# Kernel tuning notes

Measured on AMD Instinct MI355X. Metric: run time of the kernel, lower is better.

Reference implementation:

```python
import jax, jax.numpy as jnp
import numpy as np

TEMPERATURE = 0.5
NEG_FILL = -9e15


def setup_inputs() -> dict:
    key = jax.random.key(0)
    k1, k2 = jax.random.split(key)
    B, D = 8192, 128
    z1 = jax.random.normal(k1, (B, D), dtype=jnp.float32)
    z2 = jax.random.normal(k2, (B, D), dtype=jnp.float32)
    return {"z1": z1, "z2": z2}


def reference(z1, z2):
    B = z1.shape[0]
    N = 2 * B
    z = jnp.concatenate([z1, z2], axis=0)              # [N, D]
    sim = jnp.matmul(z, z.T) / TEMPERATURE             # [N, N]
    eye = jnp.eye(N, dtype=bool)
    sim = jnp.where(eye, NEG_FILL, sim)
    idx = jnp.arange(N)
    pos_idx = (idx + B) % N
    positives = sim[idx, pos_idx]                      # [N]
    loss = -positives + jax.scipy.special.logsumexp(sim, axis=1)
    return loss.mean()
```

## Files before the change

### kernel.cpp

```cpp
#include <hip/hip_runtime.h>
#include <stdint.h>


typedef __attribute__((ext_vector_type(8))) short s16x8;
typedef __attribute__((ext_vector_type(16))) float f32x16;

#define N_TOT   16384
#define NHALF   8192
#define DDIM    128
#define NQ      16
#define QW      (N_TOT / NQ)
#define BN      64
#define NT      (QW / BN)
#define BM      256
#define NRB     (N_TOT / BM)
#define CSH     128.0f
#define LN2     0.69314718055994530942f
#define BF_SCALE 1.6986436f

__device__ __forceinline__ unsigned short f2bf(float f) {
    union { float f; unsigned int u; } v; v.f = f;
    unsigned int u = v.u;
    unsigned int r = (u + 0x7FFFu + ((u >> 16) & 1u)) >> 16;
    return (unsigned short)r;
}

__device__ __forceinline__ void gload_lds16(const void* g, void* l) {
    __builtin_amdgcn_global_load_lds(
        (const __attribute__((address_space(1))) void*)g,
        (__attribute__((address_space(3))) void*)l, 16, 0, 0);
}

__global__ __launch_bounds__(256) void k_castpos(const float* __restrict__ z1,
                                                 const float* __restrict__ z2,
                                                 unsigned short* __restrict__ zb,
                                                 float* __restrict__ pos_part) {
    __shared__ float red[4];
    int i = blockIdx.x * 256 + threadIdx.x;
    float4 a = ((const float4*)z1)[i];
    float4 b = ((const float4*)z2)[i];
    ushort4 oa, ob;
    oa.x = f2bf(a.x * BF_SCALE); oa.y = f2bf(a.y * BF_SCALE);
    oa.z = f2bf(a.z * BF_SCALE); oa.w = f2bf(a.w * BF_SCALE);
    ob.x = f2bf(b.x * BF_SCALE); ob.y = f2bf(b.y * BF_SCALE);
    ob.z = f2bf(b.z * BF_SCALE); ob.w = f2bf(b.w * BF_SCALE);
    ((ushort4*)zb)[i] = oa;
    ((ushort4*)(zb + (size_t)NHALF * DDIM))[i] = ob;
    float s = a.x * b.x + a.y * b.y + a.z * b.z + a.w * b.w;
    for (int o = 32; o; o >>= 1) s += __shfl_xor(s, o);
    int lane = threadIdx.x & 63, w = threadIdx.x >> 6;
    if (lane == 0) red[w] = s;
    __syncthreads();
    if (threadIdx.x == 0) pos_part[blockIdx.x] = red[0] + red[1] + red[2] + red[3];
}

__global__ __launch_bounds__(256) void k_main(const unsigned short* __restrict__ zb,
                                              float* __restrict__ ps) {
    __shared__ s16x8 tile[2][BN * 16];

    const int tid  = threadIdx.x;
    const int lane = tid & 63;
    const int w    = tid >> 6;
    const int h    = lane >> 5;
    const int l31  = lane & 31;

    const int bid = blockIdx.x;
    const int q   = bid >> 6;
    const int rb  = bid & 63;
    const int rowB     = rb * BM + w * 64;
    const int colStart = q * QW;

    s16x8 rf0[8], rf1[8];
    {
        const s16x8* rp0 = (const s16x8*)(zb + (size_t)(rowB + l31) * DDIM);
        const s16x8* rp1 = (const s16x8*)(zb + (size_t)(rowB + 32 + l31) * DDIM);
        #pragma unroll
        for (int ks = 0; ks < 8; ++ks) { rf0[ks] = rp0[ks * 2 + h]; rf1[ks] = rp1[ks * 2 + h]; }
    }

    int soff[4];
    #pragma unroll
    for (int j = 0; j < 4; ++j) {
        int e = w * 4 + j;
        int col = e * 4 + (lane >> 4);
        int chunk = (lane & 15) ^ (col & 15);
        soff[j] = col * 256 + chunk * 16;
    }

    #pragma unroll
    for (int j = 0; j < 4; ++j)
        gload_lds16((const char*)zb + (size_t)colStart * 256 + soff[j],
                    (char*)(&tile[0][0]) + (w * 4 + j) * 1024);
    #pragma unroll
    for (int j = 0; j < 4; ++j)
        gload_lds16((const char*)zb + (size_t)(colStart + BN) * 256 + soff[j],
                    (char*)(&tile[1][0]) + (w * 4 + j) * 1024);

    float sa[4] = {0.f, 0.f, 0.f, 0.f};
    float sb[4] = {0.f, 0.f, 0.f, 0.f};

    for (int t = 0; t < NT; ++t) {
        if (t == NT - 1) asm volatile("s_waitcnt vmcnt(0)" ::: "memory");
        else             asm volatile("s_waitcnt vmcnt(4)" ::: "memory");
        __builtin_amdgcn_s_barrier();
        const int buf = t & 1;
        const int colBase = colStart + t * BN;
        #pragma unroll
        for (int sdx = 0; sdx < 2; ++sdx) {
            const int c  = sdx * 32 + l31;
            const int cx = c & 15;
            const s16x8* tb = &tile[buf][c * 16];
            s16x8 a[8];
            #pragma unroll
            for (int ks = 0; ks < 8; ++ks) a[ks] = tb[(ks * 2 + h) ^ cx];
            f32x16 acc0 = {-CSH, -CSH, -CSH, -CSH, -CSH, -CSH, -CSH, -CSH,
                           -CSH, -CSH, -CSH, -CSH, -CSH, -CSH, -CSH, -CSH};
            f32x16 acc1 = acc0;
            #pragma unroll
            for (int ks = 0; ks < 8; ++ks) {
                acc0 = __builtin_amdgcn_mfma_f32_32x32x16_bf16(a[ks], rf0[ks], acc0, 0, 0, 0);
                acc1 = __builtin_amdgcn_mfma_f32_32x32x16_bf16(a[ks], rf1[ks], acc1, 0, 0, 0);
            }
            const int cb = colBase + sdx * 32;
            if (cb == rowB) {
                #pragma unroll
                for (int r2 = 0; r2 < 16; ++r2) {
                    int crow = (r2 & 3) + 8 * (r2 >> 2) + 4 * h;
                    if (crow == l31) acc0[r2] = -1e30f;
                }
            }
            if (cb == rowB + 32) {
                #pragma unroll
                for (int r2 = 0; r2 < 16; ++r2) {
                    int crow = (r2 & 3) + 8 * (r2 >> 2) + 4 * h;
                    if (crow == l31) acc1[r2] = -1e30f;
                }
            }
            #pragma unroll
            for (int r2 = 0; r2 < 16; r2 += 4) {
                sa[0] += __builtin_amdgcn_exp2f(acc0[r2 + 0]);
                sa[1] += __builtin_amdgcn_exp2f(acc0[r2 + 1]);
                sa[2] += __builtin_amdgcn_exp2f(acc0[r2 + 2]);
                sa[3] += __builtin_amdgcn_exp2f(acc0[r2 + 3]);
                sb[0] += __builtin_amdgcn_exp2f(acc1[r2 + 0]);
                sb[1] += __builtin_amdgcn_exp2f(acc1[r2 + 1]);
                sb[2] += __builtin_amdgcn_exp2f(acc1[r2 + 2]);
                sb[3] += __builtin_amdgcn_exp2f(acc1[r2 + 3]);
            }
        }
        __builtin_amdgcn_s_barrier();
        if (t + 2 < NT) {
            #pragma unroll
            for (int j = 0; j < 4; ++j)
                gload_lds16((const char*)zb + (size_t)(colBase + 2 * BN) * 256 + soff[j],
                            (char*)(&tile[buf][0]) + (w * 4 + j) * 1024);
        }
    }

    float sA = (sa[0] + sa[1]) + (sa[2] + sa[3]);
    float sB = (sb[0] + sb[1]) + (sb[2] + sb[3]);
    sA += __shfl_xor(sA, 32);
    sB += __shfl_xor(sB, 32);
    if (lane < 32) {
        ps[(size_t)q * N_TOT + rowB + l31]      = sA;
        ps[(size_t)q * N_TOT + rowB + 32 + l31] = sB;
    }
}

__global__ __launch_bounds__(256) void k_combine(const float* __restrict__ ps,
                                                 float* __restrict__ lse_part) {
    __shared__ float red[4];
    int row = blockIdx.x * 256 + threadIdx.x;
    float s = 0.f;
    #pragma unroll
    for (int qq = 0; qq < NQ; ++qq) s += ps[(size_t)qq * N_TOT + row];
    float lse = LN2 * (CSH + log2f(s));
    for (int o = 32; o; o >>= 1) lse += __shfl_xor(lse, o);
    int lane = threadIdx.x & 63, wv = threadIdx.x >> 6;
    if (lane == 0) red[wv] = lse;
    __syncthreads();
    if (threadIdx.x == 0) lse_part[blockIdx.x] = red[0] + red[1] + red[2] + red[3];
}

__global__ void k_final(const float* __restrict__ lse_part,
                        const float* __restrict__ pos_part,
                        float* __restrict__ out) {
    __shared__ float red[4];
    int t = threadIdx.x;
    float v = (t < 64) ? lse_part[t] : 0.f;
    float p = pos_part[t] + pos_part[t + 256] + pos_part[t + 512] + pos_part[t + 768];
    float x = v - 4.0f * p;
    for (int o = 32; o; o >>= 1) x += __shfl_xor(x, o);
    int lane = t & 63, wv = t >> 6;
    if (lane == 0) red[wv] = x;
    __syncthreads();
    if (t == 0) out[0] = (red[0] + red[1] + red[2] + red[3]) * (1.0f / (float)N_TOT);
}

extern "C" void kernel_launch(void* const* d_in, const int* in_sizes, int n_in,
                              void* d_out, int out_size, void* d_ws, size_t ws_size,
                              hipStream_t stream) {
    const float* z1 = (const float*)d_in[0];
    const float* z2 = (const float*)d_in[1];
    float* out = (float*)d_out;

    char* ws = (char*)d_ws;
    float* ps       = (float*)ws;
    float* lse_part = (float*)(ws + (1u << 20));
    float* pos_part = (float*)(ws + (1u << 20) + 1024);
    unsigned short* zb = (unsigned short*)(ws + (2u << 20));

    k_castpos<<<dim3(1024), dim3(256), 0, stream>>>(z1, z2, zb, pos_part);
    k_main<<<dim3(NRB * NQ), dim3(256), 0, stream>>>(zb, ps);
    k_combine<<<dim3(N_TOT / 256), dim3(256), 0, stream>>>(ps, lse_part);
    k_final<<<dim3(1), dim3(256), 0, stream>>>(lse_part, pos_part, out);
}
```

Baseline: 136.9 us.

## Use 512-row blocks, triple-buffered LDS tiles, and fuse combine/final via atomics

```diff
diff --git a/kernel.cpp b/kernel.cpp
--- a/kernel.cpp
+++ b/kernel.cpp
@@ -12,7 +12,7 @@
 #define QW      (N_TOT / NQ)
 #define BN      64
 #define NT      (QW / BN)
-#define BM      256
+#define BM      512
 #define NRB     (N_TOT / BM)
 #define CSH     128.0f
 #define LN2     0.69314718055994530942f
@@ -34,9 +34,11 @@
 __global__ __launch_bounds__(256) void k_castpos(const float* __restrict__ z1,
                                                  const float* __restrict__ z2,
                                                  unsigned short* __restrict__ zb,
-                                                 float* __restrict__ pos_part) {
+                                                 float* __restrict__ pos_part,
+                                                 float* __restrict__ ws_acc) {
     __shared__ float red[4];
     int i = blockIdx.x * 256 + threadIdx.x;
+    if (i == 0) { ws_acc[0] = 0.f; ((unsigned int*)ws_acc)[1] = 0u; }
     float4 a = ((const float4*)z1)[i];
     float4 b = ((const float4*)z2)[i];
     ushort4 oa, ob;
@@ -54,9 +56,9 @@
     if (threadIdx.x == 0) pos_part[blockIdx.x] = red[0] + red[1] + red[2] + red[3];
 }
 
-__global__ __launch_bounds__(256) void k_main(const unsigned short* __restrict__ zb,
-                                              float* __restrict__ ps) {
-    __shared__ s16x8 tile[2][BN * 16];
+__global__ __launch_bounds__(512, 4) void k_main(const unsigned short* __restrict__ zb,
+                                                 float* __restrict__ ps) {
+    __shared__ s16x8 tile[3][BN * 16];
 
     const int tid  = threadIdx.x;
     const int lane = tid & 63;
@@ -65,8 +67,8 @@
     const int l31  = lane & 31;
 
     const int bid = blockIdx.x;
-    const int q   = bid >> 6;
-    const int rb  = bid & 63;
+    const int q   = bid >> 5;
+    const int rb  = bid & 31;
     const int rowB     = rb * BM + w * 64;
     const int colStart = q * QW;
 
@@ -78,38 +80,46 @@
         for (int ks = 0; ks < 8; ++ks) { rf0[ks] = rp0[ks * 2 + h]; rf1[ks] = rp1[ks * 2 + h]; }
     }
 
-    int soff[4];
-    #pragma unroll
-    for (int j = 0; j < 4; ++j) {
-        int e = w * 4 + j;
+    int soff[2];
+    #pragma unroll
+    for (int j = 0; j < 2; ++j) {
+        int e = w * 2 + j;
         int col = e * 4 + (lane >> 4);
         int chunk = (lane & 15) ^ (col & 15);
         soff[j] = col * 256 + chunk * 16;
     }
 
     #pragma unroll
-    for (int j = 0; j < 4; ++j)
+    for (int j = 0; j < 2; ++j)
         gload_lds16((const char*)zb + (size_t)colStart * 256 + soff[j],
-                    (char*)(&tile[0][0]) + (w * 4 + j) * 1024);
-    #pragma unroll
-    for (int j = 0; j < 4; ++j)
+                    (char*)(&tile[0][0]) + (w * 2 + j) * 1024);
+    #pragma unroll
+    for (int j = 0; j < 2; ++j)
         gload_lds16((const char*)zb + (size_t)(colStart + BN) * 256 + soff[j],
-                    (char*)(&tile[1][0]) + (w * 4 + j) * 1024);
+                    (char*)(&tile[1][0]) + (w * 2 + j) * 1024);
 
     float sa[4] = {0.f, 0.f, 0.f, 0.f};
     float sb[4] = {0.f, 0.f, 0.f, 0.f};
 
+    int bc = 0;
+    int bp = 2;
     for (int t = 0; t < NT; ++t) {
-        if (t == NT - 1) asm volatile("s_waitcnt vmcnt(0)" ::: "memory");
-        else             asm volatile("s_waitcnt vmcnt(4)" ::: "memory");
+        if (t < NT - 1) asm volatile("s_waitcnt vmcnt(2)" ::: "memory");
+        else            asm volatile("s_waitcnt vmcnt(0)" ::: "memory");
         __builtin_amdgcn_s_barrier();
-        const int buf = t & 1;
+        if (t + 2 < NT) {
+            #pragma unroll
+            for (int j = 0; j < 2; ++j)
+                gload_lds16((const char*)zb + (size_t)(colStart + (t + 2) * BN) * 256 + soff[j],
+                            (char*)(&tile[0][0]) + bp * 16384 + (w * 2 + j) * 1024);
+        }
         const int colBase = colStart + t * BN;
+        const s16x8* tbase = &tile[0][0] + bc * (BN * 16);
         #pragma unroll
         for (int sdx = 0; sdx < 2; ++sdx) {
             const int c  = sdx * 32 + l31;
             const int cx = c & 15;
-            const s16x8* tb = &tile[buf][c * 16];
+            const s16x8* tb = tbase + c * 16;
             s16x8 a[8];
             #pragma unroll
             for (int ks = 0; ks < 8; ++ks) a[ks] = tb[(ks * 2 + h) ^ cx];
@@ -148,13 +158,8 @@
                 sb[3] += __builtin_amdgcn_exp2f(acc1[r2 + 3]);
             }
         }
-        __builtin_amdgcn_s_barrier();
-        if (t + 2 < NT) {
-            #pragma unroll
-            for (int j = 0; j < 4; ++j)
-                gload_lds16((const char*)zb + (size_t)(colBase + 2 * BN) * 256 + soff[j],
-                            (char*)(&tile[buf][0]) + (w * 4 + j) * 1024);
-        }
+        bc = (bc == 2) ? 0 : bc + 1;
+        bp = (bp == 2) ? 0 : bp + 1;
     }
 
     float sA = (sa[0] + sa[1]) + (sa[2] + sa[3]);
@@ -167,34 +172,46 @@
     }
 }
 
-__global__ __launch_bounds__(256) void k_combine(const float* __restrict__ ps,
-                                                 float* __restrict__ lse_part) {
+__global__ __launch_bounds__(256) void k_cf(const float* __restrict__ ps,
+                                            const float* __restrict__ pos_part,
+                                            float* __restrict__ ws_acc,
+                                            float* __restrict__ out) {
     __shared__ float red[4];
-    int row = blockIdx.x * 256 + threadIdx.x;
-    float s = 0.f;
-    #pragma unroll
-    for (int qq = 0; qq < NQ; ++qq) s += ps[(size_t)qq * N_TOT + row];
-    float lse = LN2 * (CSH + log2f(s));
-    for (int o = 32; o; o >>= 1) lse += __shfl_xor(lse, o);
-    int lane = threadIdx.x & 63, wv = threadIdx.x >> 6;
-    if (lane == 0) red[wv] = lse;
+    __shared__ int last;
+    const int tid = threadIdx.x;
+    const int base = blockIdx.x * 1024;
+    float ls = 0.f;
+    #pragma unroll
+    for (int k = 0; k < 4; ++k) {
+        int row = base + k * 256 + tid;
+        float s = 0.f;
+        #pragma unroll
+        for (int qq = 0; qq < NQ; ++qq) s += ps[(size_t)qq * N_TOT + row];
+        ls += LN2 * (CSH + log2f(s));
+    }
+    for (int o = 32; o; o >>= 1) ls += __shfl_xor(ls, o);
+    int lane = tid & 63, wv = tid >> 6;
+    if (lane == 0) red[wv] = ls;
     __syncthreads();
-    if (threadIdx.x == 0) lse_part[blockIdx.x] = red[0] + red[1] + red[2] + red[3];
-}
-
-__global__ void k_final(const float* __restrict__ lse_part,
-                        const float* __restrict__ pos_part,
-                        float* __restrict__ out) {
-    __shared__ float red[4];
-    int t = threadIdx.x;
-    float v = (t < 64) ? lse_part[t] : 0.f;
-    float p = pos_part[t] + pos_part[t + 256] + pos_part[t + 512] + pos_part[t + 768];
-    float x = v - 4.0f * p;
-    for (int o = 32; o; o >>= 1) x += __shfl_xor(x, o);
-    int lane = t & 63, wv = t >> 6;
-    if (lane == 0) red[wv] = x;
+    if (tid == 0) {
+        atomicAdd(&ws_acc[0], red[0] + red[1] + red[2] + red[3]);
+        __threadfence();
+        unsigned int old = atomicAdd(&((unsigned int*)ws_acc)[1], 1u);
+        last = (old == 15u) ? 1 : 0;
+    }
     __syncthreads();
-    if (t == 0) out[0] = (red[0] + red[1] + red[2] + red[3]) * (1.0f / (float)N_TOT);
+    if (last) {
+        float p = pos_part[tid] + pos_part[tid + 256] +
+                  pos_part[tid + 512] + pos_part[tid + 768];
+        for (int o = 32; o; o >>= 1) p += __shfl_xor(p, o);
+        if (lane == 0) red[wv] = p;
+        __syncthreads();
+        if (tid == 0) {
+            float lse_tot = atomicAdd(&ws_acc[0], 0.f);
+            float pos_tot = red[0] + red[1] + red[2] + red[3];
+            out[0] = (lse_tot - 4.0f * pos_tot) * (1.0f / (float)N_TOT);
+        }
+    }
 }
 
 extern "C" void kernel_launch(void* const* d_in, const int* in_sizes, int n_in,
@@ -206,12 +223,11 @@
 
     char* ws = (char*)d_ws;
     float* ps       = (float*)ws;
-    float* lse_part = (float*)(ws + (1u << 20));
+    float* ws_acc   = (float*)(ws + (1u << 20));
     float* pos_part = (float*)(ws + (1u << 20) + 1024);
     unsigned short* zb = (unsigned short*)(ws + (2u << 20));
 
-    k_castpos<<<dim3(1024), dim3(256), 0, stream>>>(z1, z2, zb, pos_part);
-    k_main<<<dim3(NRB * NQ), dim3(256), 0, stream>>>(zb, ps);
-    k_combine<<<dim3(N_TOT / 256), dim3(256), 0, stream>>>(ps, lse_part);
-    k_final<<<dim3(1), dim3(256), 0, stream>>>(lse_part, pos_part, out);
-}
+    k_castpos<<<dim3(1024), dim3(256), 0, stream>>>(z1, z2, zb, pos_part, ws_acc);
+    k_main<<<dim3(NRB * NQ), dim3(512), 0, stream>>>(zb, ps);
+    k_cf<<<dim3(16), dim3(256), 0, stream>>>(ps, pos_part, ws_acc, out);
+}
```

New measurement: 322.5 us. 136% more time.
